# Kernel tuning notes

Hardware: AMD Instinct MI355X
Metric: run time of the kernel (lower is better)

Reference implementation:

```python
import jax, jax.numpy as jnp
import numpy as np

N = 2048  # device_num
K = 32    # neighbors per device


def setup_inputs() -> dict:
    key = jax.random.key(0)
    k1, k2, k3 = jax.random.split(key, 3)
    dynamic_re = jax.random.uniform(k1, (N, N), dtype=jnp.float32)
    static_re = jax.random.uniform(k2, (N,), dtype=jnp.float32)
    # neighbor ids in [0, N) excluding self (draw in [0, N-1) then shift past row index)
    r = jax.random.randint(k3, (N, K), 0, N - 1)
    rows = jnp.arange(N)[:, None]
    neighbor_matrix = (r + (r >= rows)).astype(jnp.int32)
    return {"dynamic_re": dynamic_re, "static_re": static_re, "neighbor_matrix": neighbor_matrix}


def _trust_forward(dynamic_re, static_re, neighbor_matrix):
    # Semantics of RobustTrustComputing.__call__ on a fresh instance (temp_storage empty):
    #  - diagonal: 1.0
    #  - neighbor (j in nbr(i)): history has len 1 -> CI branch is False -> combined
    #    tau = 0.7*dyn[i,j] + 0.3*stat[j]; prev==combined -> hysteresis takes the
    #    'x <= prev' path: sigmoid(combined + 0.5) with sigmoid(z)=(1-e^-z)/(1+e^-z)=tanh(z/2)
    #  - non-neighbor with common neighbors c: 0.8 * mean_c rep[i,c]*rep[c,j] read from the
    #    PARTIALLY-FILLED matrix in row-major write order (rep[i,c] nonzero only if c<j,
    #    rep[c,j] nonzero only if c<i); divisor is the FULL common-neighbor count.
    #  - non-neighbor, no common neighbors: 0.5*stat[j]
    #  - final clamp to [0,1]
    n = dynamic_re.shape[0]
    idx = jnp.arange(n)
    # membership matrix: M[i, c] True iff c appears in neighbor list of i
    M = jnp.zeros((n, n), dtype=bool).at[idx[:, None], neighbor_matrix].set(True)
    nbrval = jnp.tanh(0.5 * (0.7 * dynamic_re + 0.3 * static_re[None, :] + 0.5))
    Mf = M.astype(dynamic_re.dtype)
    count = Mf @ Mf.T                                  # |common neighbors(i, j)|
    Bmask = Mf.T * (idx[:, None] < idx[None, :])       # [c, j]: c in nbr(j) AND c < j
    fallback = 0.5 * static_re                         # [j]

    def step(rep, xs):
        i, M_i, nbr_i, cnt_i = xs
        # rep[i, c] (c in nbr(i)) equals nbrval[i, c] once column c has been written (c < j,
        # handled by Bmask); rep[c, j] is the final row c only for c < i (rows >= i are zero).
        A = jnp.where(M_i & (idx < i), nbr_i, 0.0)     # [c]
        num = jnp.einsum('c,cj,cj->j', A, rep, Bmask)  # [j]
        indirect = 0.8 * num / jnp.maximum(cnt_i, 1.0)
        row = jnp.where(M_i, nbr_i, jnp.where(cnt_i > 0, indirect, fallback))
        row = jnp.where(idx == i, 1.0, row)            # diagonal overrides everything
        return rep.at[i].set(row), None

    rep0 = jnp.zeros((n, n), dynamic_re.dtype)
    rep, _ = jax.lax.scan(step, rep0, (idx, M, nbrval, count))
    return jnp.clip(rep, 0.0, 1.0)


def reference(dynamic_re, static_re, neighbor_matrix):
    return _trust_forward(dynamic_re, static_re, neighbor_matrix)
```

## Files before the change

### kernel.cpp

```cpp
#include <hip/hip_runtime.h>
#include <math.h>
#include <limits.h>

#define WAVE 64
#define IMAX 96

__device__ __forceinline__ float nvval(float d, float s) {
    return tanhf(0.5f * (0.7f * d + 0.3f * s + 0.5f));
}
__device__ __forceinline__ float clamp01(float x) {
    return fminf(fmaxf(x, 0.0f), 1.0f);
}

__global__ void build_lists(const int* __restrict__ nbr, int N, int K, int W,
                            int* __restrict__ nbrs_sorted, int* __restrict__ deg,
                            unsigned* __restrict__ Mbits, unsigned* __restrict__ Tbits,
                            int* __restrict__ invcnt, int* __restrict__ invlist) {
    int tid = blockIdx.x * blockDim.x + threadIdx.x;
    int i = tid / WAVE;
    int lane = tid % WAVE;
    if (i >= N) return;
    bool have = (lane < K);
    int val = have ? nbr[(size_t)i * K + lane] : INT_MAX;
    bool dup = false;
    for (int t = 0; t < K; ++t) {
        int vt = __shfl(val, t);
        if (have && t < lane && vt == val) dup = true;
    }
    int dupi = (dup || !have) ? 1 : 0;
    int pos = 0;
    for (int t = 0; t < K; ++t) {
        int vt = __shfl(val, t);
        int dt = __shfl(dupi, t);
        if (!dt && vt < val) pos++;
    }
    int myp = (have && !dup) ? pos : -1;
    unsigned long long m = __ballot(have && !dup);
    int degv = __popcll(m);
    int slot = INT_MAX;
    for (int t = 0; t < K; ++t) {
        int pt = __shfl(myp, t);
        int vt = __shfl(val, t);
        if (pt == lane) slot = vt;
    }
    if (lane < K) nbrs_sorted[(size_t)i * K + lane] = slot;
    if (lane == 0) deg[i] = degv;
    if (have && !dup) {
        atomicOr(&Mbits[(size_t)i * W + (val >> 5)], 1u << (val & 31));
        atomicOr(&Tbits[(size_t)val * W + (i >> 5)], 1u << (i & 31));
        int p = atomicAdd(&invcnt[val], 1);
        if (p < IMAX) invlist[(size_t)val * IMAX + p] = i;
    } else if (have) {
        atomicOr(&Mbits[(size_t)i * W + (val >> 5)], 1u << (val & 31));
        atomicOr(&Tbits[(size_t)val * W + (i >> 5)], 1u << (i & 31));
    }
}

__global__ void phase1(const float* __restrict__ dyn, const float* __restrict__ stat,
                       const int* __restrict__ nbrs_sorted, const int* __restrict__ deg,
                       const unsigned* __restrict__ Mbits, int N, int K, int W,
                       float* __restrict__ out) {
    int tid = blockIdx.x * blockDim.x + threadIdx.x;
    int j = tid / WAVE;
    int lane = tid % WAVE;
    if (j >= N) return;
    int degj = deg[j];
    int c = (lane < K) ? nbrs_sorted[(size_t)j * K + lane] : INT_MAX;
    bool validk = (lane < degj);
    float sk = validk ? stat[c] : 0.0f;
    float statj = stat[j];
    float v = 0.0f;
    for (int m = 0; m < degj; ++m) {
        int i = __shfl(c, m);
        int b = 0;
        float term = 0.0f;
        if (validk) {
            unsigned wm = Mbits[(size_t)i * W + (c >> 5)];
            b = (wm >> (c & 31)) & 1;
            if (b && lane < m && c < j)
                term = nvval(dyn[(size_t)i * N + c], sk) * v;
        }
        int cnt = b;
        float num = term;
        for (int off = 32; off > 0; off >>= 1) {
            cnt += __shfl_xor(cnt, off);
            num += __shfl_xor(num, off);
        }
        unsigned wd = Mbits[(size_t)i * W + (j >> 5)];
        int dir = (wd >> (j & 31)) & 1;
        float val;
        if (dir) val = nvval(dyn[(size_t)i * N + j], statj);
        else if (cnt > 0) val = 0.8f * num / (float)cnt;
        else val = 0.5f * statj;
        val = clamp01(val);
        if (lane == m) v = val;
    }
    if (validk) out[(size_t)c * N + j] = v;
}

__global__ void __launch_bounds__(256) phase2(
        const float* __restrict__ dyn, const float* __restrict__ stat,
        const int* __restrict__ nbrs_sorted,
        const unsigned* __restrict__ Mbits, const unsigned* __restrict__ Tbits,
        const int* __restrict__ invcnt, const int* __restrict__ invlist,
        int N, int K, int W, float* __restrict__ out) {
    extern __shared__ char smem[];
    int* s_cnt = (int*)smem;
    float* s_num = (float*)(s_cnt + N);
    unsigned* s_Mw = (unsigned*)(s_num + N);
    unsigned* s_Sw = s_Mw + W;
    int* s_nbr = (int*)(s_Sw + W);
    float* s_nv = (float*)(s_nbr + K);
    int* s_icnt = (int*)(s_nv + K);

    int i = blockIdx.x;
    int tid = threadIdx.x;

    for (int t = tid; t < N; t += blockDim.x) { s_cnt[t] = 0; s_num[t] = 0.0f; }
    if (tid < W) {
        s_Mw[tid] = Mbits[(size_t)i * W + tid];
        s_Sw[tid] = Tbits[(size_t)i * W + tid];
    }
    if (tid < K) {
        int c = nbrs_sorted[(size_t)i * K + tid];
        s_nbr[tid] = c;
        if (c < N) {
            s_nv[tid] = nvval(dyn[(size_t)i * N + c], stat[c]);
            s_icnt[tid] = invcnt[c];
        } else {
            s_nv[tid] = 0.0f;
            s_icnt[tid] = 0;
        }
    }
    __syncthreads();

    {
        int k = tid >> 3;
        int e0 = tid & 7;
        if (k < K) {
            int c = s_nbr[k];
            int m = s_icnt[k];
            float nv = s_nv[k];
            for (int e = e0; e < m; e += 8) {
                int j = invlist[(size_t)c * IMAX + e];
                atomicAdd(&s_cnt[j], 1);
                if (c < i && c < j)
                    atomicAdd(&s_num[j], nv * out[(size_t)c * N + j]);
            }
        }
    }
    __syncthreads();

    for (int j = tid; j < N; j += blockDim.x) {
        bool skip = ((s_Sw[j >> 5] >> (j & 31)) & 1u) != 0u;
        bool dir  = ((s_Mw[j >> 5] >> (j & 31)) & 1u) != 0u;
        float val;
        if (j == i) {
            val = 1.0f;
        } else if (dir) {
            val = nvval(dyn[(size_t)i * N + j], stat[j]);
        } else {
            int cnt = s_cnt[j];
            val = (cnt > 0) ? (0.8f * s_num[j] / (float)cnt) : (0.5f * stat[j]);
        }
        val = clamp01(val);
        if (!skip) out[(size_t)i * N + j] = val;
    }
}

extern "C" void kernel_launch(void* const* d_in, const int* in_sizes, int n_in,
                              void* d_out, int out_size, void* d_ws, size_t ws_size,
                              hipStream_t stream) {
    const float* dyn = (const float*)d_in[0];
    const float* stat = (const float*)d_in[1];
    const int* nbr = (const int*)d_in[2];
    int N = in_sizes[1];
    int K = in_sizes[2] / N;
    int W = (N + 31) / 32;
    float* out = (float*)d_out;

    char* ws = (char*)d_ws;
    size_t offNbr = 0;
    size_t offDeg = offNbr + (size_t)N * K * sizeof(int);
    size_t offM = offDeg + (size_t)N * sizeof(int);
    size_t offT = offM + (size_t)N * W * sizeof(unsigned);
    size_t offIC = offT + (size_t)N * W * sizeof(unsigned);
    size_t offIL = offIC + (size_t)N * sizeof(int);
    int* nbrs_sorted = (int*)(ws + offNbr);
    int* deg = (int*)(ws + offDeg);
    unsigned* Mbits = (unsigned*)(ws + offM);
    unsigned* Tbits = (unsigned*)(ws + offT);
    int* invcnt = (int*)(ws + offIC);
    int* invlist = (int*)(ws + offIL);

    hipMemsetAsync(ws + offM, 0, offIL - offM, stream);

    int threads = 256;
    int blocksWave = (N * WAVE + threads - 1) / threads;
    build_lists<<<blocksWave, threads, 0, stream>>>(nbr, N, K, W, nbrs_sorted, deg,
                                                    Mbits, Tbits, invcnt, invlist);
    phase1<<<blocksWave, threads, 0, stream>>>(dyn, stat, nbrs_sorted, deg, Mbits,
                                               N, K, W, out);
    size_t smem = (size_t)N * 8 + (size_t)W * 8 + (size_t)K * 12;
    phase2<<<N, threads, smem, stream>>>(dyn, stat, nbrs_sorted, Mbits, Tbits,
                                         invcnt, invlist, N, K, W, out);
}
```

Baseline: 133.1 us.

## Hoist phase1 loads out of the sequential neighbor recurrence into LDS precompute

Phase1 previously performed dependent global loads (membership bits, dyn values) and full 64-lane reductions inside the serial per-neighbor loop. The new code precomputes membership bitmasks, direct-edge values via the transpose bitmap, common-neighbor counts via ballots, and the nvval products into per-wave shared memory, leaving only a 32-lane shuffle reduction in the serial chain. It skips reductions entirely for steps with no contributing terms. It also clamps the inverse-list count to IMAX in phase2 for safety, and assumes K<=32 (KMAX).

```diff
diff --git a/kernel.cpp b/kernel.cpp
--- a/kernel.cpp
+++ b/kernel.cpp
@@ -3,6 +3,7 @@
 #include <limits.h>
 
 #define WAVE 64
+#define KMAX 32
 #define IMAX 96
 
 __device__ __forceinline__ float nvval(float d, float s) {
@@ -45,52 +46,87 @@
     }
     if (lane < K) nbrs_sorted[(size_t)i * K + lane] = slot;
     if (lane == 0) deg[i] = degv;
-    if (have && !dup) {
+    if (have) {
         atomicOr(&Mbits[(size_t)i * W + (val >> 5)], 1u << (val & 31));
         atomicOr(&Tbits[(size_t)val * W + (i >> 5)], 1u << (i & 31));
-        int p = atomicAdd(&invcnt[val], 1);
-        if (p < IMAX) invlist[(size_t)val * IMAX + p] = i;
-    } else if (have) {
-        atomicOr(&Mbits[(size_t)i * W + (val >> 5)], 1u << (val & 31));
-        atomicOr(&Tbits[(size_t)val * W + (i >> 5)], 1u << (i & 31));
-    }
-}
-
-__global__ void phase1(const float* __restrict__ dyn, const float* __restrict__ stat,
-                       const int* __restrict__ nbrs_sorted, const int* __restrict__ deg,
-                       const unsigned* __restrict__ Mbits, int N, int K, int W,
-                       float* __restrict__ out) {
+        if (!dup) {
+            int p = atomicAdd(&invcnt[val], 1);
+            if (p < IMAX) invlist[(size_t)val * IMAX + p] = i;
+        }
+    }
+}
+
+__global__ void __launch_bounds__(256) phase1(
+        const float* __restrict__ dyn, const float* __restrict__ stat,
+        const int* __restrict__ nbrs_sorted, const int* __restrict__ deg,
+        const unsigned* __restrict__ Mbits, const unsigned* __restrict__ Tbits,
+        int N, int K, int W, float* __restrict__ out) {
+    __shared__ float s_nv[4 * KMAX * KMAX];
     int tid = blockIdx.x * blockDim.x + threadIdx.x;
     int j = tid / WAVE;
-    int lane = tid % WAVE;
+    int lane = threadIdx.x & (WAVE - 1);
+    int waveid = threadIdx.x >> 6;
     if (j >= N) return;
     int degj = deg[j];
     int c = (lane < K) ? nbrs_sorted[(size_t)j * K + lane] : INT_MAX;
     bool validk = (lane < degj);
     float sk = validk ? stat[c] : 0.0f;
     float statj = stat[j];
+    float* s_row = &s_nv[waveid * KMAX * KMAX];
+
+    unsigned dirbit = 0;
+    if (validk) {
+        unsigned w = Tbits[(size_t)j * W + (c >> 5)];
+        dirbit = (w >> (c & 31)) & 1u;
+    }
+    unsigned dirmask = (unsigned)__ballot(dirbit != 0);
+    float dv = 0.0f;
+    if (dirbit) dv = nvval(dyn[(size_t)c * N + j], statj);
+
+    unsigned hmAll = 0;
+    #pragma unroll
+    for (int m = 0; m < KMAX; ++m) {
+        int cm = __shfl(c, m);
+        if (cm < N) {
+            unsigned w = validk ? Mbits[(size_t)cm * W + (c >> 5)] : 0u;
+            unsigned b = (w >> (c & 31)) & 1u;
+            hmAll |= b << m;
+            if (b && lane < m && c < j)
+                s_row[m * KMAX + lane] = nvval(dyn[(size_t)cm * N + c], sk);
+        }
+    }
+    unsigned lm = (lane < 31) ? (0xFFFFFFFEu << lane) : 0u;
+    unsigned hmTerm = (validk && c < j) ? (hmAll & lm) : 0u;
+
+    int mycnt = 0;
+    unsigned H = 0;
+    #pragma unroll
+    for (int m = 0; m < KMAX; ++m) {
+        unsigned long long ball = __ballot((hmAll >> m) & 1u);
+        unsigned long long ballT = __ballot((hmTerm >> m) & 1u);
+        if (lane == m) mycnt = __popcll(ball);
+        H |= (ballT ? 1u : 0u) << m;
+    }
+    H = __builtin_amdgcn_readfirstlane(H);
+    dirmask = __builtin_amdgcn_readfirstlane(dirmask);
+
     float v = 0.0f;
-    for (int m = 0; m < degj; ++m) {
-        int i = __shfl(c, m);
-        int b = 0;
-        float term = 0.0f;
-        if (validk) {
-            unsigned wm = Mbits[(size_t)i * W + (c >> 5)];
-            b = (wm >> (c & 31)) & 1;
-            if (b && lane < m && c < j)
-                term = nvval(dyn[(size_t)i * N + c], sk) * v;
-        }
-        int cnt = b;
-        float num = term;
-        for (int off = 32; off > 0; off >>= 1) {
-            cnt += __shfl_xor(cnt, off);
-            num += __shfl_xor(num, off);
-        }
-        unsigned wd = Mbits[(size_t)i * W + (j >> 5)];
-        int dir = (wd >> (j & 31)) & 1;
+    #pragma unroll
+    for (int m = 0; m < KMAX; ++m) {
+        float num = 0.0f;
+        if (H & (1u << m)) {
+            float t = 0.0f;
+            if ((hmTerm >> m) & 1u) t = s_row[m * KMAX + lane] * v;
+            num = t;
+            num += __shfl_xor(num, 16);
+            num += __shfl_xor(num, 8);
+            num += __shfl_xor(num, 4);
+            num += __shfl_xor(num, 2);
+            num += __shfl_xor(num, 1);
+        }
         float val;
-        if (dir) val = nvval(dyn[(size_t)i * N + j], statj);
-        else if (cnt > 0) val = 0.8f * num / (float)cnt;
+        if ((dirmask >> m) & 1u) val = dv;
+        else if (mycnt > 0) val = 0.8f * num / (float)mycnt;
         else val = 0.5f * statj;
         val = clamp01(val);
         if (lane == m) v = val;
@@ -126,7 +162,8 @@
         s_nbr[tid] = c;
         if (c < N) {
             s_nv[tid] = nvval(dyn[(size_t)i * N + c], stat[c]);
-            s_icnt[tid] = invcnt[c];
+            int m = invcnt[c];
+            s_icnt[tid] = (m < IMAX) ? m : IMAX;
         } else {
             s_nv[tid] = 0.0f;
             s_icnt[tid] = 0;
@@ -199,8 +236,8 @@
     int blocksWave = (N * WAVE + threads - 1) / threads;
     build_lists<<<blocksWave, threads, 0, stream>>>(nbr, N, K, W, nbrs_sorted, deg,
                                                     Mbits, Tbits, invcnt, invlist);
-    phase1<<<blocksWave, threads, 0, stream>>>(dyn, stat, nbrs_sorted, deg, Mbits,
-                                               N, K, W, out);
+    phase1<<<blocksWave, threads, 0, stream>>>(dyn, stat, nbrs_sorted, deg,
+                                               Mbits, Tbits, N, K, W, out);
     size_t smem = (size_t)N * 8 + (size_t)W * 8 + (size_t)K * 12;
     phase2<<<N, threads, smem, stream>>>(dyn, stat, nbrs_sorted, Mbits, Tbits,
                                          invcnt, invlist, N, K, W, out);
```

Result: faster. 127.6 us (-4.1%).
